# Performance work log

Hardware: AMD Instinct MI355X
Metric: run time of the kernel (lower is better)

Reference implementation:

```python
import jax, jax.numpy as jnp
import numpy as np
import math

B = 128
STRIDES = (8.0, 16.0, 32.0)
GRIDS = (128, 64, 32)
C_Q = 4
LAMBDA_BBOX = 5.0
LAMBDA_QUALITY = 0.05
FOCAL_ALPHA = 0.25
FOCAL_GAMMA = 2.0
EPS = 1e-6


def setup_inputs() -> dict:
    key = jax.random.key(0)
    ks = jax.random.split(key, 12)
    inp = {}
    for i, (hw, name) in enumerate(zip(GRIDS, ('det_map8', 'det_map16', 'det_map32'))):
        inp[name] = jax.random.normal(ks[i], (B, 5, hw, hw), dtype=jnp.float32)
    for i, (hw, name) in enumerate(zip(GRIDS, ('qual_map8', 'qual_map16', 'qual_map32'))):
        inp[name] = jax.random.normal(ks[3 + i], (B, C_Q, hw, hw), dtype=jnp.float32)
    # realistic GT boxes inside a 1024x1024 image; every 16th sample invalid (x1 < 0)
    x1 = jax.random.uniform(ks[6], (B,), minval=0.0, maxval=600.0)
    y1 = jax.random.uniform(ks[7], (B,), minval=0.0, maxval=600.0)
    w = jax.random.uniform(ks[8], (B,), minval=64.0, maxval=320.0)
    h = jax.random.uniform(ks[9], (B,), minval=64.0, maxval=320.0)
    boxes = jnp.stack([x1, y1, jnp.minimum(x1 + w, 1023.0), jnp.minimum(y1 + h, 1023.0)], axis=1)
    invalid = (jnp.arange(B) % 16) == 0
    boxes = jnp.where(invalid[:, None], -1.0, boxes)
    inp['gt_bboxes'] = boxes.astype(jnp.float32)
    inp['gt_quality'] = jax.random.uniform(ks[10], (B, C_Q), dtype=jnp.float32)
    return inp


def _level_losses(det, qual, stride, gt_bboxes, gt_quality, valid):
    Bn, _, H, W = det.shape
    gy, gx = jnp.meshgrid(jnp.arange(H, dtype=jnp.float32),
                          jnp.arange(W, dtype=jnp.float32), indexing='ij')
    cx = (gx + 0.5) * stride  # [H,W]
    cy = (gy + 0.5) * stride
    x1 = gt_bboxes[:, 0, None, None]
    y1 = gt_bboxes[:, 1, None, None]
    x2 = gt_bboxes[:, 2, None, None]
    y2 = gt_bboxes[:, 3, None, None]
    in_box = (cx > x1) & (cx < x2) & (cy > y1) & (cy < y2) & valid[:, None, None]  # [B,H,W]

    # --- focal loss on conf channel ---
    z = det[:, 0]
    t = in_box.astype(jnp.float32)
    ce = jnp.maximum(z, 0.0) - z * t + jnp.log1p(jnp.exp(-jnp.abs(z)))
    p = jax.nn.sigmoid(z)
    pt = jnp.where(t == 1, p, 1.0 - p)
    a_t = jnp.where(t == 1, FOCAL_ALPHA, 1.0 - FOCAL_ALPHA)
    focal = a_t * (1.0 - pt) ** FOCAL_GAMMA * ce
    conf = (focal * valid[:, None, None].astype(jnp.float32)).mean()

    # --- CIoU on positive cells (vectorized, masked) ---
    pl = jnp.exp(jnp.clip(det[:, 1], -6.0, 6.0)) * stride
    pt_ = jnp.exp(jnp.clip(det[:, 2], -6.0, 6.0)) * stride
    pr = jnp.exp(jnp.clip(det[:, 3], -6.0, 6.0)) * stride
    pb = jnp.exp(jnp.clip(det[:, 4], -6.0, 6.0)) * stride
    # safe GT distances: positive dummy outside the mask to avoid NaN poisoning
    gl = jnp.where(in_box, cx - x1, 1.0)
    gtl = jnp.where(in_box, cy - y1, 1.0)
    gr = jnp.where(in_box, x2 - cx, 1.0)
    gb = jnp.where(in_box, y2 - cy, 1.0)
    pw = pl + pr
    ph = pt_ + pb
    gw = gl + gr
    gh = gtl + gb
    iw = jnp.clip(jnp.minimum(pl, gl) + jnp.minimum(pr, gr), 0.0)
    ih = jnp.clip(jnp.minimum(pt_, gtl) + jnp.minimum(pb, gb), 0.0)
    inter = iw * ih
    union = pw * ph + gw * gh - inter + EPS
    iou = inter / union
    c_w = jnp.maximum(pl, gl) + jnp.maximum(pr, gr)
    c_h = jnp.maximum(pt_, gtl) + jnp.maximum(pb, gb)
    c2 = c_w ** 2 + c_h ** 2 + EPS
    dcx = (pr - pl) / 2.0 - (gr - gl) / 2.0
    dcy = (pb - pt_) / 2.0 - (gb - gtl) / 2.0
    rho2 = dcx ** 2 + dcy ** 2
    v = (4.0 / math.pi ** 2) * (jnp.arctan(gw / (gh + EPS)) - jnp.arctan(pw / (ph + EPS))) ** 2
    alpha_v = jax.lax.stop_gradient(v / (1.0 - iou + v + EPS))
    ciou = 1.0 - iou + rho2 / c2 + alpha_v * v  # [B,H,W]
    npos_b = in_box.sum(axis=(1, 2))  # [B]
    ciou_mean = (ciou * t).sum(axis=(1, 2)) / jnp.maximum(npos_b, 1).astype(jnp.float32)
    has_pos = npos_b > 0
    bbox = jnp.where(has_pos, ciou_mean, 0.0).sum()

    # --- quality BCE at the positive cell closest to box center ---
    bcx = (gt_bboxes[:, 0] + gt_bboxes[:, 2]) / 2.0
    bcy = (gt_bboxes[:, 1] + gt_bboxes[:, 3]) / 2.0
    dist2 = (cx - bcx[:, None, None]) ** 2 + (cy - bcy[:, None, None]) ** 2
    dist2 = jnp.where(in_box, dist2, jnp.inf)
    idx = jnp.argmin(dist2.reshape(Bn, -1), axis=1)  # [B]
    qual_flat = qual.reshape(Bn, qual.shape[1], -1)  # [B,Cq,HW]
    best = jnp.take_along_axis(qual_flat, idx[:, None, None], axis=2)[:, :, 0]  # [B,Cq]
    q_tgt = jnp.clip(gt_quality, 0.05, 0.95)
    bce = -(q_tgt * jax.nn.log_sigmoid(best) + (1.0 - q_tgt) * jax.nn.log_sigmoid(-best))
    qual_loss = jnp.where(has_pos, bce.mean(axis=1), 0.0).sum()

    return conf, bbox, qual_loss, has_pos.sum()


def _stage_a_loss(det_maps, qual_maps, gt_bboxes, gt_quality):
    valid = gt_bboxes[:, 0] >= 0
    total_conf = jnp.float32(0.0)
    total_bbox = jnp.float32(0.0)
    total_qual = jnp.float32(0.0)
    n_pos = jnp.int32(0)
    for det, qual, stride in zip(det_maps, qual_maps, STRIDES):
        c, b_, q, n = _level_losses(det, qual, stride, gt_bboxes, gt_quality, valid)
        total_conf = total_conf + c
        total_bbox = total_bbox + b_
        total_qual = total_qual + q
        n_pos = n_pos + n
    denom = jnp.maximum(n_pos, 1).astype(jnp.float32)
    total_bbox = jnp.where(n_pos > 0, total_bbox / denom, total_bbox)
    total_qual = jnp.where(n_pos > 0, total_qual / denom, total_qual)
    total = total_conf + LAMBDA_BBOX * total_bbox + LAMBDA_QUALITY * total_qual
    return total, total_conf, total_bbox, total_qual


def reference(det_map8, det_map16, det_map32, qual_map8, qual_map16, qual_map32,
              gt_bboxes, gt_quality):
    return _stage_a_loss((det_map8, det_map16, det_map32),
                         (qual_map8, qual_map16, qual_map32),
                         gt_bboxes, gt_quality)
```

## Files before the change

### kernel.cpp

```cpp
#include <hip/hip_runtime.h>
#include <math.h>


#define NBLK 768

__device__ __forceinline__ float rcpf(float x) { return __builtin_amdgcn_rcpf(x); }

__device__ __forceinline__ float logsigf(float x) {
    return fminf(x, 0.f) - __logf(1.f + __expf(-fabsf(x)));
}

__device__ __forceinline__ void ciou_one(
    float cx, float cy, float stride, float ls, float ts, float rs, float bs,
    float x1, float y1, float x2, float y2, float bcx, float bcy, int locj,
    float& ciou, int& np, unsigned long long& pk)
{
    const float pl  = __expf(fminf(fmaxf(ls, -6.f), 6.f)) * stride;
    const float pt_ = __expf(fminf(fmaxf(ts, -6.f), 6.f)) * stride;
    const float pr  = __expf(fminf(fmaxf(rs, -6.f), 6.f)) * stride;
    const float pb  = __expf(fminf(fmaxf(bs, -6.f), 6.f)) * stride;
    const float gl  = cx - x1, gtl = cy - y1, gr = x2 - cx, gb = y2 - cy;
    const float pw = pl + pr, ph = pt_ + pb;
    const float gw = gl + gr, gh = gtl + gb;
    const float iw = fmaxf(fminf(pl, gl) + fminf(pr, gr), 0.f);
    const float ih = fmaxf(fminf(pt_, gtl) + fminf(pb, gb), 0.f);
    const float inter = iw * ih;
    const float uni   = pw * ph + gw * gh - inter + 1e-6f;
    const float iou   = inter * rcpf(uni);
    const float cw_ = fmaxf(pl, gl) + fmaxf(pr, gr);
    const float ch_ = fmaxf(pt_, gtl) + fmaxf(pb, gb);
    const float c2  = cw_ * cw_ + ch_ * ch_ + 1e-6f;
    const float dcx = 0.5f * (pr - pl) - 0.5f * (gr - gl);
    const float dcy = 0.5f * (pb - pt_) - 0.5f * (gb - gtl);
    const float rho2 = dcx * dcx + dcy * dcy;
    const float dv = atanf(gw * rcpf(gh + 1e-6f)) - atanf(pw * rcpf(ph + 1e-6f));
    const float v  = (4.f / (float)(M_PI * M_PI)) * dv * dv;
    const float alpha = v * rcpf(1.f - iou + v + 1e-6f);
    ciou += 1.f - iou + rho2 * rcpf(c2) + alpha * v;
    ++np;
    const float ddx = cx - bcx, ddy = cy - bcy;
    const float dist2 = ddx * ddx + ddy * ddy;
    const unsigned long long cand =
        ((unsigned long long)__float_as_uint(dist2) << 32) | (unsigned)locj;
    pk = cand < pk ? cand : pk;
}

__device__ __forceinline__ void focal4(const float4& d0, const bool inb[4], float& conf)
{
    const float zs[4] = { d0.x, d0.y, d0.z, d0.w };
    #pragma unroll
    for (int j = 0; j < 4; ++j) {
        const float z  = zs[j];
        const float e  = __expf(-fabsf(z));
        const float ce = fmaxf(z, 0.f) - (inb[j] ? z : 0.f) + __logf(1.f + e);
        const float inv = rcpf(1.f + e);
        const float p  = (z >= 0.f) ? inv : e * inv;
        const float pt = inb[j] ? p : 1.f - p;
        const float at = inb[j] ? 0.25f : 0.75f;
        const float om = 1.f - pt;
        conf += at * om * om * ce;
    }
}

__global__ __launch_bounds__(256) void level_k(
    const float* __restrict__ det8, const float* __restrict__ det16, const float* __restrict__ det32,
    const float* __restrict__ q16, const float* __restrict__ q32,
    const float* __restrict__ gtb, const float* __restrict__ gtq,
    unsigned long long* __restrict__ pk_p, float* __restrict__ conf_part,
    float* __restrict__ ciou_p, int* __restrict__ np_p,
    float* __restrict__ bbox_c, float* __restrict__ qual_c, int* __restrict__ npf)
{
    const int tid = (int)threadIdx.x;
    const int bid = (int)blockIdx.x;

    int b, base, log2W, nstripe;
    const float* det; float stride; float inv_denom; size_t HW;
    if (bid < 512) {
        b = bid >> 2; base = (bid & 3) * 4096; nstripe = 4;
        det = det8;  stride = 8.f;  log2W = 7; HW = 16384; inv_denom = 1.f / 2097152.f;
    } else if (bid < 640) {
        b = bid - 512; base = 0; nstripe = 4;
        det = det16; stride = 16.f; log2W = 6; HW = 4096; inv_denom = 1.f / 524288.f;
    } else {
        b = bid - 640; base = 0; nstripe = 1;
        det = det32; stride = 32.f; log2W = 5; HW = 1024; inv_denom = 1.f / 131072.f;
    }

    float conf = 0.f, ciou = 0.f; int np = 0;
    unsigned long long pk = ~0ULL;

    const float x1 = gtb[b * 4 + 0];
    if (x1 >= 0.f) {
        const float y1 = gtb[b * 4 + 1];
        const float x2 = gtb[b * 4 + 2];
        const float y2 = gtb[b * 4 + 3];
        const float bcx = 0.5f * (x1 + x2);
        const float bcy = 0.5f * (y1 + y2);
        const size_t c0base = (size_t)(b * 5) * HW;
        const int Wm1 = (1 << log2W) - 1;
        const int loc0 = base + (tid << 2);

        const int xi = loc0 & Wm1;
        float cxs[4]; bool cxok[4];
        #pragma unroll
        for (int j = 0; j < 4; ++j) {
            cxs[j]  = ((float)(xi + j) + 0.5f) * stride;
            cxok[j] = (cxs[j] > x1) & (cxs[j] < x2);
        }
        const float dcy = stride * (float)(1024 >> log2W);
        float cy = ((float)(loc0 >> log2W) + 0.5f) * stride;

        if (nstripe == 4) {
            float4 d[4];
            #pragma unroll
            for (int s = 0; s < 4; ++s)
                d[s] = *(const float4*)(det + c0base + (size_t)(loc0 + s * 1024));
            #pragma unroll
            for (int s = 0; s < 4; ++s) {
                const int loc = loc0 + s * 1024;
                const bool cyok = (cy > y1) & (cy < y2);
                bool inb[4]; bool anyb = false;
                #pragma unroll
                for (int j = 0; j < 4; ++j) { inb[j] = cxok[j] & cyok; anyb |= inb[j]; }
                focal4(d[s], inb, conf);
                if (__any(anyb)) {
                    const float4 d1 = *(const float4*)(det + c0base + HW + (size_t)loc);
                    const float4 d2 = *(const float4*)(det + c0base + 2 * HW + (size_t)loc);
                    const float4 d3 = *(const float4*)(det + c0base + 3 * HW + (size_t)loc);
                    const float4 d4 = *(const float4*)(det + c0base + 4 * HW + (size_t)loc);
                    const float ls[4] = { d1.x, d1.y, d1.z, d1.w };
                    const float ts[4] = { d2.x, d2.y, d2.z, d2.w };
                    const float rs[4] = { d3.x, d3.y, d3.z, d3.w };
                    const float bs[4] = { d4.x, d4.y, d4.z, d4.w };
                    #pragma unroll
                    for (int j = 0; j < 4; ++j)
                        if (inb[j])
                            ciou_one(cxs[j], cy, stride, ls[j], ts[j], rs[j], bs[j],
                                     x1, y1, x2, y2, bcx, bcy, loc + j, ciou, np, pk);
                }
                cy += dcy;
            }
        } else {
            const float4 d0 = *(const float4*)(det + c0base + (size_t)loc0);
            const bool cyok = (cy > y1) & (cy < y2);
            bool inb[4]; bool anyb = false;
            #pragma unroll
            for (int j = 0; j < 4; ++j) { inb[j] = cxok[j] & cyok; anyb |= inb[j]; }
            focal4(d0, inb, conf);
            if (__any(anyb)) {
                const float4 d1 = *(const float4*)(det + c0base + HW + (size_t)loc0);
                const float4 d2 = *(const float4*)(det + c0base + 2 * HW + (size_t)loc0);
                const float4 d3 = *(const float4*)(det + c0base + 3 * HW + (size_t)loc0);
                const float4 d4 = *(const float4*)(det + c0base + 4 * HW + (size_t)loc0);
                const float ls[4] = { d1.x, d1.y, d1.z, d1.w };
                const float ts[4] = { d2.x, d2.y, d2.z, d2.w };
                const float rs[4] = { d3.x, d3.y, d3.z, d3.w };
                const float bs[4] = { d4.x, d4.y, d4.z, d4.w };
                #pragma unroll
                for (int j = 0; j < 4; ++j)
                    if (inb[j])
                        ciou_one(cxs[j], cy, stride, ls[j], ts[j], rs[j], bs[j],
                                 x1, y1, x2, y2, bcx, bcy, loc0 + j, ciou, np, pk);
            }
        }
        conf *= inv_denom;
    }

    #pragma unroll
    for (int off = 32; off > 0; off >>= 1) {
        conf += __shfl_down(conf, off);
        ciou += __shfl_down(ciou, off);
        np   += __shfl_down(np, off);
        unsigned long long o = __shfl_down(pk, off);
        pk = o < pk ? o : pk;
    }

    __shared__ float s_conf[4], s_ciou[4];
    __shared__ int   s_np[4];
    __shared__ unsigned long long s_pk[4];
    const int wid = tid >> 6;
    if ((tid & 63) == 0) {
        s_conf[wid] = conf; s_ciou[wid] = ciou; s_np[wid] = np; s_pk[wid] = pk;
    }
    __syncthreads();
    if (tid == 0) {
        conf_part[bid] = s_conf[0] + s_conf[1] + s_conf[2] + s_conf[3];
        const float ci = s_ciou[0] + s_ciou[1] + s_ciou[2] + s_ciou[3];
        const int   nt = s_np[0] + s_np[1] + s_np[2] + s_np[3];
        unsigned long long mn = s_pk[0];
        mn = s_pk[1] < mn ? s_pk[1] : mn;
        mn = s_pk[2] < mn ? s_pk[2] : mn;
        mn = s_pk[3] < mn ? s_pk[3] : mn;
        if (bid < 512) {
            ciou_p[bid] = ci; np_p[bid] = nt; pk_p[bid] = mn;
        } else {
            const int e = bid - 512;
            float bbv = 0.f, qlv = 0.f; int flag = 0;
            if (nt > 0) {
                bbv = ci * rcpf((float)nt);
                const unsigned idx = (unsigned)(mn & 0xffffffffULL);
                const float* q = (bid < 640) ? q16 : q32;
                const int l2  = (bid < 640) ? 12 : 10;
                float s = 0.f;
                #pragma unroll
                for (int c = 0; c < 4; ++c) {
                    const float best = q[((size_t)(b * 4 + c) << l2) + idx];
                    const float qt = fminf(fmaxf(gtq[b * 4 + c], 0.05f), 0.95f);
                    s -= qt * logsigf(best) + (1.f - qt) * logsigf(-best);
                }
                qlv = 0.25f * s;
                flag = 1;
            }
            bbox_c[e] = bbv; qual_c[e] = qlv; npf[e] = flag;
        }
    }
}

__global__ __launch_bounds__(512) void fin_k(
    const float* __restrict__ q8, const float* __restrict__ gtq,
    const unsigned long long* __restrict__ pk_p, const float* __restrict__ conf_part,
    const float* __restrict__ ciou_p, const int* __restrict__ np_p,
    const float* __restrict__ bbox_c, const float* __restrict__ qual_c,
    const int* __restrict__ npf,
    float* __restrict__ out)
{
    const int i = threadIdx.x;
    __shared__ unsigned sidx[128];

    float cp = 0.f;
    if (i < 192) {
        const float4 v = ((const float4*)conf_part)[i];
        cp = v.x + v.y + v.z + v.w;
    }

    float bb = 0.f, ql = 0.f; int n = 0;

    if (i < 128) {
        const float4 cv = *(const float4*)(ciou_p + i * 4);
        const int4   nv = *(const int4*)(np_p + i * 4);
        const ulonglong2 p0 = *(const ulonglong2*)(pk_p + i * 4);
        const ulonglong2 p1 = *(const ulonglong2*)(pk_p + i * 4 + 2);
        const float ci = cv.x + cv.y + cv.z + cv.w;
        const int   np = nv.x + nv.y + nv.z + nv.w;
        unsigned long long mn = p0.x;
        mn = p0.y < mn ? p0.y : mn;
        mn = p1.x < mn ? p1.x : mn;
        mn = p1.y < mn ? p1.y : mn;
        if (np > 0) {
            bb += ci * rcpf((float)np);
            n  += 1;
            sidx[i] = (unsigned)(mn & 0xffffffffULL);
        } else {
            sidx[i] = 0xFFFFFFFFu;
        }
    } else if (i < 384) {
        const int e = i - 128;
        bb += bbox_c[e]; ql += qual_c[e]; n += npf[e];
    }
    __syncthreads();

    {
        const int s = i >> 2, c = i & 3;
        const unsigned idx = sidx[s];
        float term = 0.f;
        if (idx != 0xFFFFFFFFu) {
            const float best = q8[((size_t)(s * 4 + c) << 14) + idx];
            const float qt = fminf(fmaxf(gtq[s * 4 + c], 0.05f), 0.95f);
            term = -(qt * logsigf(best) + (1.f - qt) * logsigf(-best));
        }
        term += __shfl_down(term, 2);
        term += __shfl_down(term, 1);
        if (c == 0) ql += 0.25f * term;
    }

    #pragma unroll
    for (int off = 32; off > 0; off >>= 1) {
        cp += __shfl_down(cp, off);
        bb += __shfl_down(bb, off);
        ql += __shfl_down(ql, off);
        n  += __shfl_down(n, off);
    }
    __shared__ float wc[8], wb[8], wq[8];
    __shared__ int   wn[8];
    if ((i & 63) == 0) { wc[i >> 6] = cp; wb[i >> 6] = bb; wq[i >> 6] = ql; wn[i >> 6] = n; }
    __syncthreads();
    if (i == 0) {
        float conf_t = 0.f, tb0 = 0.f, tq0 = 0.f; int ntot = 0;
        #pragma unroll
        for (int w = 0; w < 8; ++w) { conf_t += wc[w]; tb0 += wb[w]; tq0 += wq[w]; ntot += wn[w]; }
        const float denom = fmaxf((float)ntot, 1.f);
        const float tb = (ntot > 0) ? tb0 / denom : tb0;
        const float tq = (ntot > 0) ? tq0 / denom : tq0;
        out[0] = conf_t + 5.f * tb + 0.05f * tq;
        out[1] = conf_t;
        out[2] = tb;
        out[3] = tq;
    }
}

extern "C" void kernel_launch(void* const* d_in, const int* in_sizes, int n_in,
                              void* d_out, int out_size, void* d_ws, size_t ws_size,
                              hipStream_t stream) {
    const float* det8  = (const float*)d_in[0];
    const float* det16 = (const float*)d_in[1];
    const float* det32 = (const float*)d_in[2];
    const float* q8    = (const float*)d_in[3];
    const float* q16   = (const float*)d_in[4];
    const float* q32   = (const float*)d_in[5];
    const float* gtb   = (const float*)d_in[6];
    const float* gtq   = (const float*)d_in[7];
    float* out = (float*)d_out;

    unsigned long long* pk_p = (unsigned long long*)d_ws;
    float* conf_part = (float*)((char*)d_ws + 4096);
    float* ciou_p    = (float*)((char*)d_ws + 7168);
    int*   np_p      = (int*)((char*)d_ws + 9216);
    float* bbox_c    = (float*)((char*)d_ws + 11264);
    float* qual_c    = (float*)((char*)d_ws + 12288);
    int*   npf       = (int*)((char*)d_ws + 13312);

    hipLaunchKernelGGL(level_k, dim3(NBLK), dim3(256), 0, stream,
                       det8, det16, det32, q16, q32, gtb, gtq,
                       pk_p, conf_part, ciou_p, np_p, bbox_c, qual_c, npf);
    hipLaunchKernelGGL(fin_k, dim3(1), dim3(512), 0, stream,
                       q8, gtq, pk_p, conf_part, ciou_p, np_p, bbox_c, qual_c, npf, out);
}
```

Before: 21.30 us.

## Use one 1024-thread block per sample per level and fold quality gather into it

```diff
diff --git a/kernel.cpp b/kernel.cpp
--- a/kernel.cpp
+++ b/kernel.cpp
@@ -2,7 +2,7 @@
 #include <math.h>
 
 
-#define NBLK 768
+#define NBLK 384
 
 __device__ __forceinline__ float rcpf(float x) { return __builtin_amdgcn_rcpf(x); }
 
@@ -62,35 +62,63 @@
     }
 }
 
-__global__ __launch_bounds__(256) void level_k(
+__device__ __forceinline__ void stripe4(
+    const float* __restrict__ det, size_t c0base, int loc, size_t HW, float stride,
+    const float cxs[4], const bool cxok[4], float cy,
+    float x1, float y1, float x2, float y2, float bcx, float bcy,
+    const float4& d0, float& conf, float& ciou, int& np, unsigned long long& pk)
+{
+    const bool cyok = (cy > y1) & (cy < y2);
+    bool inb[4]; bool anyb = false;
+    #pragma unroll
+    for (int j = 0; j < 4; ++j) { inb[j] = cxok[j] & cyok; anyb |= inb[j]; }
+    focal4(d0, inb, conf);
+    if (__any(anyb)) {
+        const float4 d1 = *(const float4*)(det + c0base + HW + (size_t)loc);
+        const float4 d2 = *(const float4*)(det + c0base + 2 * HW + (size_t)loc);
+        const float4 d3 = *(const float4*)(det + c0base + 3 * HW + (size_t)loc);
+        const float4 d4 = *(const float4*)(det + c0base + 4 * HW + (size_t)loc);
+        const float ls[4] = { d1.x, d1.y, d1.z, d1.w };
+        const float ts[4] = { d2.x, d2.y, d2.z, d2.w };
+        const float rs[4] = { d3.x, d3.y, d3.z, d3.w };
+        const float bs[4] = { d4.x, d4.y, d4.z, d4.w };
+        #pragma unroll
+        for (int j = 0; j < 4; ++j)
+            if (inb[j])
+                ciou_one(cxs[j], cy, stride, ls[j], ts[j], rs[j], bs[j],
+                         x1, y1, x2, y2, bcx, bcy, loc + j, ciou, np, pk);
+    }
+}
+
+__global__ __launch_bounds__(1024) void level_k(
     const float* __restrict__ det8, const float* __restrict__ det16, const float* __restrict__ det32,
-    const float* __restrict__ q16, const float* __restrict__ q32,
+    const float* __restrict__ q8, const float* __restrict__ q16, const float* __restrict__ q32,
     const float* __restrict__ gtb, const float* __restrict__ gtq,
-    unsigned long long* __restrict__ pk_p, float* __restrict__ conf_part,
-    float* __restrict__ ciou_p, int* __restrict__ np_p,
-    float* __restrict__ bbox_c, float* __restrict__ qual_c, int* __restrict__ npf)
+    float4* __restrict__ contrib)
 {
     const int tid = (int)threadIdx.x;
     const int bid = (int)blockIdx.x;
 
-    int b, base, log2W, nstripe;
-    const float* det; float stride; float inv_denom; size_t HW;
-    if (bid < 512) {
-        b = bid >> 2; base = (bid & 3) * 4096; nstripe = 4;
-        det = det8;  stride = 8.f;  log2W = 7; HW = 16384; inv_denom = 1.f / 2097152.f;
-    } else if (bid < 640) {
-        b = bid - 512; base = 0; nstripe = 4;
-        det = det16; stride = 16.f; log2W = 6; HW = 4096; inv_denom = 1.f / 524288.f;
+    int b, log2W, l2q, nstripe;
+    const float* det; const float* q; float stride; float inv_denom; size_t HW;
+    bool active = true;
+    if (bid < 128) {
+        b = bid; det = det8; q = q8;
+        stride = 8.f;  log2W = 7; HW = 16384; l2q = 14; nstripe = 4; inv_denom = 1.f / 2097152.f;
+    } else if (bid < 256) {
+        b = bid - 128; det = det16; q = q16;
+        stride = 16.f; log2W = 6; HW = 4096;  l2q = 12; nstripe = 1; inv_denom = 1.f / 524288.f;
     } else {
-        b = bid - 640; base = 0; nstripe = 1;
-        det = det32; stride = 32.f; log2W = 5; HW = 1024; inv_denom = 1.f / 131072.f;
+        b = bid - 256; det = det32; q = q32;
+        stride = 32.f; log2W = 5; HW = 1024;  l2q = 10; nstripe = 1; inv_denom = 1.f / 131072.f;
+        active = (tid < 256);
     }
 
     float conf = 0.f, ciou = 0.f; int np = 0;
     unsigned long long pk = ~0ULL;
 
     const float x1 = gtb[b * 4 + 0];
-    if (x1 >= 0.f) {
+    if (x1 >= 0.f && active) {
         const float y1 = gtb[b * 4 + 1];
         const float x2 = gtb[b * 4 + 2];
         const float y2 = gtb[b * 4 + 3];
@@ -98,7 +126,7 @@
         const float bcy = 0.5f * (y1 + y2);
         const size_t c0base = (size_t)(b * 5) * HW;
         const int Wm1 = (1 << log2W) - 1;
-        const int loc0 = base + (tid << 2);
+        const int loc0 = tid << 2;
 
         const int xi = loc0 & Wm1;
         float cxs[4]; bool cxok[4];
@@ -107,61 +135,24 @@
             cxs[j]  = ((float)(xi + j) + 0.5f) * stride;
             cxok[j] = (cxs[j] > x1) & (cxs[j] < x2);
         }
-        const float dcy = stride * (float)(1024 >> log2W);
         float cy = ((float)(loc0 >> log2W) + 0.5f) * stride;
 
         if (nstripe == 4) {
+            const float dcy = stride * (float)(4096 >> log2W);
             float4 d[4];
             #pragma unroll
             for (int s = 0; s < 4; ++s)
-                d[s] = *(const float4*)(det + c0base + (size_t)(loc0 + s * 1024));
+                d[s] = *(const float4*)(det + c0base + (size_t)(loc0 + s * 4096));
             #pragma unroll
             for (int s = 0; s < 4; ++s) {
-                const int loc = loc0 + s * 1024;
-                const bool cyok = (cy > y1) & (cy < y2);
-                bool inb[4]; bool anyb = false;
-                #pragma unroll
-                for (int j = 0; j < 4; ++j) { inb[j] = cxok[j] & cyok; anyb |= inb[j]; }
-                focal4(d[s], inb, conf);
-                if (__any(anyb)) {
-                    const float4 d1 = *(const float4*)(det + c0base + HW + (size_t)loc);
-                    const float4 d2 = *(const float4*)(det + c0base + 2 * HW + (size_t)loc);
-                    const float4 d3 = *(const float4*)(det + c0base + 3 * HW + (size_t)loc);
-                    const float4 d4 = *(const float4*)(det + c0base + 4 * HW + (size_t)loc);
-                    const float ls[4] = { d1.x, d1.y, d1.z, d1.w };
-                    const float ts[4] = { d2.x, d2.y, d2.z, d2.w };
-                    const float rs[4] = { d3.x, d3.y, d3.z, d3.w };
-                    const float bs[4] = { d4.x, d4.y, d4.z, d4.w };
-                    #pragma unroll
-                    for (int j = 0; j < 4; ++j)
-                        if (inb[j])
-                            ciou_one(cxs[j], cy, stride, ls[j], ts[j], rs[j], bs[j],
-                                     x1, y1, x2, y2, bcx, bcy, loc + j, ciou, np, pk);
-                }
+                stripe4(det, c0base, loc0 + s * 4096, HW, stride, cxs, cxok, cy,
+                        x1, y1, x2, y2, bcx, bcy, d[s], conf, ciou, np, pk);
                 cy += dcy;
             }
         } else {
             const float4 d0 = *(const float4*)(det + c0base + (size_t)loc0);
-            const bool cyok = (cy > y1) & (cy < y2);
-            bool inb[4]; bool anyb = false;
-            #pragma unroll
-            for (int j = 0; j < 4; ++j) { inb[j] = cxok[j] & cyok; anyb |= inb[j]; }
-            focal4(d0, inb, conf);
-            if (__any(anyb)) {
-                const float4 d1 = *(const float4*)(det + c0base + HW + (size_t)loc0);
-                const float4 d2 = *(const float4*)(det + c0base + 2 * HW + (size_t)loc0);
-                const float4 d3 = *(const float4*)(det + c0base + 3 * HW + (size_t)loc0);
-                const float4 d4 = *(const float4*)(det + c0base + 4 * HW + (size_t)loc0);
-                const float ls[4] = { d1.x, d1.y, d1.z, d1.w };
-                const float ts[4] = { d2.x, d2.y, d2.z, d2.w };
-                const float rs[4] = { d3.x, d3.y, d3.z, d3.w };
-                const float bs[4] = { d4.x, d4.y, d4.z, d4.w };
-                #pragma unroll
-                for (int j = 0; j < 4; ++j)
-                    if (inb[j])
-                        ciou_one(cxs[j], cy, stride, ls[j], ts[j], rs[j], bs[j],
-                                 x1, y1, x2, y2, bcx, bcy, loc0 + j, ciou, np, pk);
-            }
+            stripe4(det, c0base, loc0, HW, stride, cxs, cxok, cy,
+                    x1, y1, x2, y2, bcx, bcy, d0, conf, ciou, np, pk);
         }
         conf *= inv_denom;
     }
@@ -175,119 +166,64 @@
         pk = o < pk ? o : pk;
     }
 
-    __shared__ float s_conf[4], s_ciou[4];
-    __shared__ int   s_np[4];
-    __shared__ unsigned long long s_pk[4];
+    __shared__ float s_conf[16], s_ciou[16];
+    __shared__ int   s_np[16];
+    __shared__ unsigned long long s_pk[16];
     const int wid = tid >> 6;
     if ((tid & 63) == 0) {
         s_conf[wid] = conf; s_ciou[wid] = ciou; s_np[wid] = np; s_pk[wid] = pk;
     }
     __syncthreads();
     if (tid == 0) {
-        conf_part[bid] = s_conf[0] + s_conf[1] + s_conf[2] + s_conf[3];
-        const float ci = s_ciou[0] + s_ciou[1] + s_ciou[2] + s_ciou[3];
-        const int   nt = s_np[0] + s_np[1] + s_np[2] + s_np[3];
-        unsigned long long mn = s_pk[0];
-        mn = s_pk[1] < mn ? s_pk[1] : mn;
-        mn = s_pk[2] < mn ? s_pk[2] : mn;
-        mn = s_pk[3] < mn ? s_pk[3] : mn;
-        if (bid < 512) {
-            ciou_p[bid] = ci; np_p[bid] = nt; pk_p[bid] = mn;
-        } else {
-            const int e = bid - 512;
-            float bbv = 0.f, qlv = 0.f; int flag = 0;
-            if (nt > 0) {
-                bbv = ci * rcpf((float)nt);
-                const unsigned idx = (unsigned)(mn & 0xffffffffULL);
-                const float* q = (bid < 640) ? q16 : q32;
-                const int l2  = (bid < 640) ? 12 : 10;
-                float s = 0.f;
-                #pragma unroll
-                for (int c = 0; c < 4; ++c) {
-                    const float best = q[((size_t)(b * 4 + c) << l2) + idx];
-                    const float qt = fminf(fmaxf(gtq[b * 4 + c], 0.05f), 0.95f);
-                    s -= qt * logsigf(best) + (1.f - qt) * logsigf(-best);
-                }
-                qlv = 0.25f * s;
-                flag = 1;
+        float cf = 0.f, ci = 0.f; int nt = 0;
+        unsigned long long mn = ~0ULL;
+        #pragma unroll
+        for (int w = 0; w < 16; ++w) {
+            cf += s_conf[w]; ci += s_ciou[w]; nt += s_np[w];
+            mn = s_pk[w] < mn ? s_pk[w] : mn;
+        }
+        float bbv = 0.f, qlv = 0.f, flag = 0.f;
+        if (nt > 0) {
+            bbv = ci * rcpf((float)nt);
+            const unsigned idx = (unsigned)(mn & 0xffffffffULL);
+            float s = 0.f;
+            #pragma unroll
+            for (int c = 0; c < 4; ++c) {
+                const float best = q[((size_t)(b * 4 + c) << l2q) + idx];
+                const float qt = fminf(fmaxf(gtq[b * 4 + c], 0.05f), 0.95f);
+                s -= qt * logsigf(best) + (1.f - qt) * logsigf(-best);
             }
-            bbox_c[e] = bbv; qual_c[e] = qlv; npf[e] = flag;
-        }
+            qlv = 0.25f * s;
+            flag = 1.f;
+        }
+        contrib[bid] = make_float4(cf, bbv, qlv, flag);
     }
 }
 
 __global__ __launch_bounds__(512) void fin_k(
-    const float* __restrict__ q8, const float* __restrict__ gtq,
-    const unsigned long long* __restrict__ pk_p, const float* __restrict__ conf_part,
-    const float* __restrict__ ciou_p, const int* __restrict__ np_p,
-    const float* __restrict__ bbox_c, const float* __restrict__ qual_c,
-    const int* __restrict__ npf,
-    float* __restrict__ out)
+    const float4* __restrict__ contrib, float* __restrict__ out)
 {
     const int i = threadIdx.x;
-    __shared__ unsigned sidx[128];
-
-    float cp = 0.f;
-    if (i < 192) {
-        const float4 v = ((const float4*)conf_part)[i];
-        cp = v.x + v.y + v.z + v.w;
-    }
-
-    float bb = 0.f, ql = 0.f; int n = 0;
-
-    if (i < 128) {
-        const float4 cv = *(const float4*)(ciou_p + i * 4);
-        const int4   nv = *(const int4*)(np_p + i * 4);
-        const ulonglong2 p0 = *(const ulonglong2*)(pk_p + i * 4);
-        const ulonglong2 p1 = *(const ulonglong2*)(pk_p + i * 4 + 2);
-        const float ci = cv.x + cv.y + cv.z + cv.w;
-        const int   np = nv.x + nv.y + nv.z + nv.w;
-        unsigned long long mn = p0.x;
-        mn = p0.y < mn ? p0.y : mn;
-        mn = p1.x < mn ? p1.x : mn;
-        mn = p1.y < mn ? p1.y : mn;
-        if (np > 0) {
-            bb += ci * rcpf((float)np);
-            n  += 1;
-            sidx[i] = (unsigned)(mn & 0xffffffffULL);
-        } else {
-            sidx[i] = 0xFFFFFFFFu;
-        }
-    } else if (i < 384) {
-        const int e = i - 128;
-        bb += bbox_c[e]; ql += qual_c[e]; n += npf[e];
-    }
-    __syncthreads();
-
-    {
-        const int s = i >> 2, c = i & 3;
-        const unsigned idx = sidx[s];
-        float term = 0.f;
-        if (idx != 0xFFFFFFFFu) {
-            const float best = q8[((size_t)(s * 4 + c) << 14) + idx];
-            const float qt = fminf(fmaxf(gtq[s * 4 + c], 0.05f), 0.95f);
-            term = -(qt * logsigf(best) + (1.f - qt) * logsigf(-best));
-        }
-        term += __shfl_down(term, 2);
-        term += __shfl_down(term, 1);
-        if (c == 0) ql += 0.25f * term;
-    }
-
+    float cf = 0.f, bb = 0.f, ql = 0.f, nf = 0.f;
+    if (i < NBLK) {
+        const float4 v = contrib[i];
+        cf = v.x; bb = v.y; ql = v.z; nf = v.w;
+    }
     #pragma unroll
     for (int off = 32; off > 0; off >>= 1) {
-        cp += __shfl_down(cp, off);
+        cf += __shfl_down(cf, off);
         bb += __shfl_down(bb, off);
         ql += __shfl_down(ql, off);
-        n  += __shfl_down(n, off);
-    }
-    __shared__ float wc[8], wb[8], wq[8];
-    __shared__ int   wn[8];
-    if ((i & 63) == 0) { wc[i >> 6] = cp; wb[i >> 6] = bb; wq[i >> 6] = ql; wn[i >> 6] = n; }
+        nf += __shfl_down(nf, off);
+    }
+    __shared__ float wc[8], wb[8], wq[8], wn[8];
+    if ((i & 63) == 0) { wc[i >> 6] = cf; wb[i >> 6] = bb; wq[i >> 6] = ql; wn[i >> 6] = nf; }
     __syncthreads();
     if (i == 0) {
-        float conf_t = 0.f, tb0 = 0.f, tq0 = 0.f; int ntot = 0;
-        #pragma unroll
-        for (int w = 0; w < 8; ++w) { conf_t += wc[w]; tb0 += wb[w]; tq0 += wq[w]; ntot += wn[w]; }
+        float conf_t = 0.f, tb0 = 0.f, tq0 = 0.f, nsum = 0.f;
+        #pragma unroll
+        for (int w = 0; w < 8; ++w) { conf_t += wc[w]; tb0 += wb[w]; tq0 += wq[w]; nsum += wn[w]; }
+        const int ntot = (int)(nsum + 0.5f);
         const float denom = fmaxf((float)ntot, 1.f);
         const float tb = (ntot > 0) ? tb0 / denom : tb0;
         const float tq = (ntot > 0) ? tq0 / denom : tq0;
@@ -311,17 +247,10 @@
     const float* gtq   = (const float*)d_in[7];
     float* out = (float*)d_out;
 
-    unsigned long long* pk_p = (unsigned long long*)d_ws;
-    float* conf_part = (float*)((char*)d_ws + 4096);
-    float* ciou_p    = (float*)((char*)d_ws + 7168);
-    int*   np_p      = (int*)((char*)d_ws + 9216);
-    float* bbox_c    = (float*)((char*)d_ws + 11264);
-    float* qual_c    = (float*)((char*)d_ws + 12288);
-    int*   npf       = (int*)((char*)d_ws + 13312);
-
-    hipLaunchKernelGGL(level_k, dim3(NBLK), dim3(256), 0, stream,
-                       det8, det16, det32, q16, q32, gtb, gtq,
-                       pk_p, conf_part, ciou_p, np_p, bbox_c, qual_c, npf);
+    float4* contrib = (float4*)d_ws;
+
+    hipLaunchKernelGGL(level_k, dim3(NBLK), dim3(1024), 0, stream,
+                       det8, det16, det32, q8, q16, q32, gtb, gtq, contrib);
     hipLaunchKernelGGL(fin_k, dim3(1), dim3(512), 0, stream,
-                       q8, gtq, pk_p, conf_part, ciou_p, np_p, bbox_c, qual_c, npf, out);
-}
+                       contrib, out);
+}
```

After: 18.19 us. -14.6%, faster.
